# Performance work log

Hardware: AMD Instinct MI355X
Metric: run time of the kernel (lower is better)

The kernel has to match this reference:

```python
import jax, jax.numpy as jnp
import numpy as np

D_MODEL = 1024
H = 16
D_HEAD = D_MODEL // H
MASK_VAL = -1e30


def setup_inputs() -> dict:
    key = jax.random.key(0)
    ks = jax.random.split(key, 10)
    B, S = 2, 2048
    scale = 1.0 / np.sqrt(D_MODEL)
    return {
        "query": jax.random.normal(ks[0], (B, S, D_MODEL), jnp.float32),
        "key": jax.random.normal(ks[1], (B, S, D_MODEL), jnp.float32),
        "value": jax.random.normal(ks[2], (B, S, D_MODEL), jnp.float32),
        "mask": jax.random.randint(ks[3], (B, S, S), 0, 2) > 0,
        "Wq": jax.random.normal(ks[4], (D_MODEL, D_MODEL), jnp.float32) * scale,
        "bq": jnp.zeros((D_MODEL,), jnp.float32),
        "Wk": jax.random.normal(ks[5], (D_MODEL, D_MODEL), jnp.float32) * scale,
        "bk": jnp.zeros((D_MODEL,), jnp.float32),
        "Wv": jax.random.normal(ks[6], (D_MODEL, D_MODEL), jnp.float32) * scale,
        "bv": jnp.zeros((D_MODEL,), jnp.float32),
    }


def _split_heads(x, B, S):
    # [B,S,D] -> [B,H,S,Dh]
    return x.reshape(B, S, H, D_HEAD).transpose(0, 2, 1, 3)


def reference(query, key, value, mask, Wq, bq, Wk, bk, Wv, bv):
    B, S, _ = query.shape
    q = _split_heads(query @ Wq.T + bq, B, S)
    k = _split_heads(key @ Wk.T + bk, B, S)
    v = _split_heads(value @ Wv.T + bv, B, S)
    # scale by sqrt of per-head dim (query.size(-1) after split)
    q = q / jnp.sqrt(jnp.asarray(D_HEAD, q.dtype))
    scores = jnp.einsum("bhqd,bhkd->bhqk", q, k)
    scores = jnp.where(mask[:, None, :, :], MASK_VAL, scores)
    attn = jax.nn.softmax(scores, axis=-1)
    out = jnp.einsum("bhqk,bhkd->bhqd", attn, v)
    return out.transpose(0, 2, 1, 3).reshape(B, S, D_MODEL)
```

## Files before the change

### kernel.cpp

```cpp
#include <hip/hip_runtime.h>
#include <hip/hip_bf16.h>

#define D_MODEL 1024
#define NH 16
#define DH 64
#define S_LEN 2048
#define BATCH 2
#define QSCALE (0.125f * 1.44269504088896f)

#define KV_HSTRIDE (S_LEN * DH)
#define WS_V_OFF   (NH * KV_HSTRIDE)
#define KVB_WORDS  (2 * NH * KV_HSTRIDE)
#define MB_WORDS   ((S_LEN / 64) * S_LEN)
#define KTILE 128
#define NT (S_LEN / KTILE)
#define X_ELEMS (BATCH * S_LEN * D_MODEL)
#define W_ELEMS (D_MODEL * D_MODEL)
#define KSTR 88

typedef __attribute__((ext_vector_type(8))) short bf16x8;
typedef __attribute__((ext_vector_type(4))) float f32x4;

static __device__ inline unsigned short f2bf(float f) {
    union { float f; unsigned u; } v; v.f = f;
    unsigned r = v.u + 0x7fffu + ((v.u >> 16) & 1u);
    return (unsigned short)(r >> 16);
}
static __device__ inline unsigned cvt2(float a, float b) {
    union { __hip_bfloat162 h2; unsigned u; } cv;
    cv.h2 = __float22bfloat162_rn(make_float2(a, b));
    return cv.u;
}
static __device__ inline bf16x8 pack8(f32x4 a, f32x4 b) {
    union { bf16x8 v; unsigned u[4]; } r;
    r.u[0] = cvt2(a[0], a[1]); r.u[1] = cvt2(a[2], a[3]);
    r.u[2] = cvt2(b[0], b[1]); r.u[3] = cvt2(b[2], b[3]);
    return r.v;
}
static __device__ inline bf16x8 cvt8(const float* __restrict__ p) {
    return pack8(*(const f32x4*)p, *(const f32x4*)(p + 4));
}
static __device__ inline float exp2_fast(float x) {
#if __has_builtin(__builtin_amdgcn_exp2f)
    return __builtin_amdgcn_exp2f(x);
#else
    return exp2f(x);
#endif
}
static __device__ inline void gload_lds16(const unsigned short* __restrict__ g,
                                          unsigned short* l, int lane) {
#if __has_builtin(__builtin_amdgcn_global_load_lds)
    __builtin_amdgcn_global_load_lds(
        (const __attribute__((address_space(1))) void*)g,
        (__attribute__((address_space(3))) void*)l, 16, 0, 0);
#else
    *(bf16x8*)((char*)l + lane * 16) = *(const bf16x8*)g;
#endif
}
static __device__ inline int vperm(int s) {
    return (s & ~31) | ((s & 12) << 1) | ((s & 16) >> 2) | (s & 3);
}

__global__ __launch_bounds__(256) void cvt_kernel(
    const float* __restrict__ q, const float* __restrict__ k,
    const float* __restrict__ v,
    const float* __restrict__ Wq, const float* __restrict__ Wk,
    const float* __restrict__ Wv,
    unsigned short* __restrict__ xb, unsigned short* __restrict__ wb)
{
    const int by = blockIdx.y;
    const float* src;
    unsigned short* dst;
    int t;
    if (blockIdx.x < 1024) {
        src = by == 0 ? q : (by == 1 ? k : v);
        dst = xb + (size_t)by * X_ELEMS;
        t = blockIdx.x * 256 + threadIdx.x;
    } else {
        src = by == 0 ? Wq : (by == 1 ? Wk : Wv);
        dst = wb + (size_t)by * W_ELEMS;
        t = (blockIdx.x - 1024) * 256 + threadIdx.x;
    }
    const size_t o = (size_t)t * 16;
    *(bf16x8*)&dst[o]     = cvt8(src + o);
    *(bf16x8*)&dst[o + 8] = cvt8(src + o + 8);
}

__global__ __launch_bounds__(256) void pack_mask_kernel(
    const int* __restrict__ mask, unsigned long long* __restrict__ mbits,
    int b_base)
{
    const int w    = blockIdx.x * 4 + (threadIdx.x >> 6);
    const int lane = threadIdx.x & 63;
    const int b    = b_base + (w >> 16);
    const int rem  = w & 65535;
    const int kt   = rem >> 11;
    const int s    = rem & 2047;
    const int v = mask[((size_t)b * S_LEN + s) * S_LEN + kt * 64 + lane];
    const unsigned long long bits = __ballot(v != 0);
    if (lane == 0) mbits[w] = bits;
}

__global__ __launch_bounds__(256) void proj_v2_kernel(
    const unsigned short* __restrict__ xb, const unsigned short* __restrict__ wb,
    const float* __restrict__ bq, const float* __restrict__ bk,
    const float* __restrict__ bv,
    float* __restrict__ q_out, unsigned short* __restrict__ ws)
{
    const int bx = blockIdx.x;
    const int by = blockIdx.y;
    const int z  = by >> 3;
    const int c0 = (by & 7) * 128;

    const unsigned short* A  = xb + (size_t)z * X_ELEMS;
    const unsigned short* Bw = wb + (size_t)z * W_ELEMS;
    const float* bias = z == 0 ? bq : (z == 1 ? bk : bv);

    const int tid  = threadIdx.x;
    const int wave = tid >> 6;
    const int lane = tid & 63;
    const int quad = lane >> 4;
    const int l16  = lane & 15;
    const int m0   = (wave & 1) * 64;
    const int n0   = (wave >> 1) * 64;

    __shared__ __align__(16) unsigned short As[128 * 32];
    __shared__ __align__(16) unsigned short Bs[128 * 32];

    const int r_lo = wave * 16 + (lane >> 2);
    const int r_hi = (wave + 4) * 16 + (lane >> 2);
    const int segu = (lane & 3) * 8;
    const int row0 = bx * 128;

    f32x4 acc[4][4] = {};

    for (int kk = 0; kk < D_MODEL; kk += 32) {
        gload_lds16(A  + (size_t)(row0 + r_lo) * D_MODEL + kk + segu, &As[wave * 512], lane);
        gload_lds16(A  + (size_t)(row0 + r_hi) * D_MODEL + kk + segu, &As[(wave + 4) * 512], lane);
        gload_lds16(Bw + (size_t)(c0 + r_lo) * D_MODEL + kk + segu, &Bs[wave * 512], lane);
        gload_lds16(Bw + (size_t)(c0 + r_hi) * D_MODEL + kk + segu, &Bs[(wave + 4) * 512], lane);
        __syncthreads();

        bf16x8 af[4], bfr[4];
#pragma unroll
        for (int i = 0; i < 4; ++i)
            af[i] = *(const bf16x8*)&As[(m0 + i * 16 + l16) * 32 + quad * 8];
#pragma unroll
        for (int j = 0; j < 4; ++j)
            bfr[j] = *(const bf16x8*)&Bs[(n0 + j * 16 + l16) * 32 + quad * 8];
#pragma unroll
        for (int i = 0; i < 4; ++i)
#pragma unroll
            for (int j = 0; j < 4; ++j)
                acc[i][j] = __builtin_amdgcn_mfma_f32_16x16x32_bf16(
                    af[i], bfr[j], acc[i][j], 0, 0, 0);
        __syncthreads();
    }

#pragma unroll
    for (int j = 0; j < 4; ++j) {
        const int cl  = c0 + n0 + j * 16 + l16;
        const float bval = bias[cl];
        const int h  = cl >> 6;
        const int dh = cl & 63;
#pragma unroll
        for (int i = 0; i < 4; ++i) {
#pragma unroll
            for (int r = 0; r < 4; ++r) {
                const int row = row0 + m0 + i * 16 + quad * 4 + r;
                const float v = acc[i][j][r] + bval;
                if (z == 0) {
                    q_out[(size_t)row * D_MODEL + cl] = v * QSCALE;
                } else {
                    unsigned short* slab = ws + (size_t)(row >> 11) * KVB_WORDS;
                    const int s = row & 2047;
                    if (z == 1)
                        slab[(size_t)h * KV_HSTRIDE + s * DH + dh] = f2bf(v);
                    else
                        slab[WS_V_OFF + (size_t)h * KV_HSTRIDE + dh * S_LEN + vperm(s)] = f2bf(v);
                }
            }
        }
    }
}

__global__ __launch_bounds__(256) void proj_fb_kernel(
    const float* __restrict__ q_in, const float* __restrict__ k_in,
    const float* __restrict__ v_in,
    const float* __restrict__ Wq, const float* __restrict__ bq,
    const float* __restrict__ Wk, const float* __restrict__ bk,
    const float* __restrict__ Wv, const float* __restrict__ bv,
    float* __restrict__ q_out, unsigned short* __restrict__ ws, int b_base)
{
    const int bx = blockIdx.x;
    const int by = blockIdx.y;
    const int z  = by >> 3;
    const int c0 = (by & 7) * 128;

    const float* x    = z == 0 ? q_in : (z == 1 ? k_in : v_in);
    const float* W    = z == 0 ? Wq   : (z == 1 ? Wk   : Wv);
    const float* bias = z == 0 ? bq   : (z == 1 ? bk   : bv);

    const int tid  = threadIdx.x;
    const int wave = tid >> 6;
    const int lane = tid & 63;
    const int quad = lane >> 4;
    const int l16  = lane & 15;
    const int m0   = (wave & 1) * 64;
    const int n0   = (wave >> 1) * 64;

    __shared__ __align__(16) unsigned short As[128][40];
    __shared__ __align__(16) unsigned short Bs[128][40];

    const int srow = tid >> 1;
    const int kcol = (tid & 1) * 16;
    const int row0 = b_base * S_LEN + bx * 128;
    const float* ag = x + (size_t)(row0 + srow) * D_MODEL + kcol;
    const float* bg = W + (size_t)(c0 + srow) * D_MODEL + kcol;

    f32x4 acc[4][4] = {};

    for (int kk = 0; kk < D_MODEL; kk += 32) {
        {
            f32x4 a0 = *(const f32x4*)(ag + kk);
            f32x4 a1 = *(const f32x4*)(ag + kk + 4);
            f32x4 a2 = *(const f32x4*)(ag + kk + 8);
            f32x4 a3 = *(const f32x4*)(ag + kk + 12);
            f32x4 b0 = *(const f32x4*)(bg + kk);
            f32x4 b1 = *(const f32x4*)(bg + kk + 4);
            f32x4 b2 = *(const f32x4*)(bg + kk + 8);
            f32x4 b3 = *(const f32x4*)(bg + kk + 12);
            *(bf16x8*)&As[srow][kcol]     = pack8(a0, a1);
            *(bf16x8*)&As[srow][kcol + 8] = pack8(a2, a3);
            *(bf16x8*)&Bs[srow][kcol]     = pack8(b0, b1);
            *(bf16x8*)&Bs[srow][kcol + 8] = pack8(b2, b3);
        }
        __syncthreads();

        bf16x8 af[4], bfr[4];
#pragma unroll
        for (int i = 0; i < 4; ++i)
            af[i] = *(const bf16x8*)&As[m0 + i * 16 + l16][quad * 8];
#pragma unroll
        for (int j = 0; j < 4; ++j)
            bfr[j] = *(const bf16x8*)&Bs[n0 + j * 16 + l16][quad * 8];
#pragma unroll
        for (int i = 0; i < 4; ++i)
#pragma unroll
            for (int j = 0; j < 4; ++j)
                acc[i][j] = __builtin_amdgcn_mfma_f32_16x16x32_bf16(
                    af[i], bfr[j], acc[i][j], 0, 0, 0);
        __syncthreads();
    }

#pragma unroll
    for (int j = 0; j < 4; ++j) {
        const int cl  = c0 + n0 + j * 16 + l16;
        const float bval = bias[cl];
        const int h  = cl >> 6;
        const int dh = cl & 63;
#pragma unroll
        for (int i = 0; i < 4; ++i) {
#pragma unroll
            for (int r = 0; r < 4; ++r) {
                const int row = row0 + m0 + i * 16 + quad * 4 + r;
                const float v = acc[i][j][r] + bval;
                if (z == 0) {
                    q_out[(size_t)row * D_MODEL + cl] = v * QSCALE;
                } else {
                    const int b_rel = (row >> 11) - b_base;
                    const int s     = row & 2047;
                    unsigned short* slab = ws + (size_t)b_rel * KVB_WORDS;
                    if (z == 1)
                        slab[(size_t)h * KV_HSTRIDE + s * DH + dh] = f2bf(v);
                    else
                        slab[WS_V_OFF + (size_t)h * KV_HSTRIDE + dh * S_LEN + vperm(s)] = f2bf(v);
                }
            }
        }
    }
}

__global__ __launch_bounds__(256) void attn_kernel(
    const unsigned short* __restrict__ ws,
    const unsigned long long* __restrict__ mbits,
    const int* __restrict__ mask,
    float* __restrict__ out, int b_base, int use_bits)
{
    const int h     = blockIdx.x;
    const int qtile = blockIdx.y;
    const int bz    = blockIdx.z;
    const int b0    = b_base + bz;

    const unsigned short* K  = ws + (size_t)bz * KVB_WORDS + (size_t)h * KV_HSTRIDE;
    const unsigned short* Vg = K + WS_V_OFF;
    const unsigned long long* mb = mbits + (size_t)bz * MB_WORDS;

    const int tid  = threadIdx.x;
    const int wave = tid >> 6;
    const int lane = tid & 63;
    const int quad = lane >> 4;
    const int l16  = lane & 15;
    const int q0   = qtile * 128;

    __shared__ __align__(16) unsigned short Vt[64][136];
    __shared__ __align__(16) unsigned short Kt[128 * KSTR];

    bf16x8 aq0a, aq1a, aq0b, aq1b;
    {
        const float* qa =
            out + (size_t)(b0 * S_LEN + q0 + wave * 16 + l16) * D_MODEL + h * DH;
        const float* qb = qa + (size_t)64 * D_MODEL;
        aq0a = cvt8(qa + quad * 8);  aq1a = cvt8(qa + 32 + quad * 8);
        aq0b = cvt8(qb + quad * 8);  aq1b = cvt8(qb + 32 + quad * 8);
    }

    const int qg = q0 + wave * 16 + l16;
    float l_a = 0.f, l_b = 0.f;
    f32x4 o_a[4] = {}, o_b[4] = {};

    const int krow = tid >> 1, kc = (tid & 1) * 32;
    const int vrow = tid >> 2, vc = (tid & 3) * 32;
    bf16x8 kr[4], vr[4];
    {
        const unsigned short* kp = K + (size_t)krow * DH + kc;
        const unsigned short* vp = Vg + (size_t)vrow * S_LEN + vc;
#pragma unroll
        for (int i = 0; i < 4; ++i) {
            kr[i] = *(const bf16x8*)(kp + 8 * i);
            vr[i] = *(const bf16x8*)(vp + 8 * i);
        }
    }

    for (int kt = 0; kt < NT; ++kt) {
#pragma unroll
        for (int i = 0; i < 4; ++i) {
            *(bf16x8*)&Kt[krow * KSTR + kc + 8 * i] = kr[i];
            *(bf16x8*)&Vt[vrow][vc + 8 * i]         = vr[i];
        }
        __syncthreads();

        if (kt + 1 < NT) {
            const unsigned short* kp = K + (size_t)((kt + 1) * KTILE + krow) * DH + kc;
            const unsigned short* vp = Vg + (size_t)vrow * S_LEN + (kt + 1) * KTILE + vc;
#pragma unroll
            for (int i = 0; i < 4; ++i) {
                kr[i] = *(const bf16x8*)(kp + 8 * i);
                vr[i] = *(const bf16x8*)(vp + 8 * i);
            }
        }

        unsigned long long wm0a = 0ull, wm1a = 0ull, wm0b = 0ull, wm1b = 0ull;
        if (use_bits) {
            wm0a = mb[(size_t)(2 * kt) * S_LEN + qg] >> (quad * 4);
            wm1a = mb[(size_t)(2 * kt + 1) * S_LEN + qg] >> (quad * 4);
            wm0b = mb[(size_t)(2 * kt) * S_LEN + qg + 64] >> (quad * 4);
            wm1b = mb[(size_t)(2 * kt + 1) * S_LEN + qg + 64] >> (quad * 4);
        }

        bf16x8 af_a[4], af_b[4];
#pragma unroll
        for (int c = 0; c < 4; ++c) {
            f32x4 sa[2], sb[2];
#pragma unroll
            for (int j = 0; j < 2; ++j) {
                const int blk = 2 * c + j;
                const unsigned short* kb = &Kt[(blk * 16 + l16) * KSTR];
                bf16x8 k0 = *(const bf16x8*)&kb[quad * 8];
                bf16x8 k1 = *(const bf16x8*)&kb[32 + quad * 8];
                f32x4 z = {0.f, 0.f, 0.f, 0.f};
                sa[j] = __builtin_amdgcn_mfma_f32_16x16x32_bf16(k0, aq0a, z, 0, 0, 0);
                sa[j] = __builtin_amdgcn_mfma_f32_16x16x32_bf16(k1, aq1a, sa[j], 0, 0, 0);
                sb[j] = __builtin_amdgcn_mfma_f32_16x16x32_bf16(k0, aq0b, z, 0, 0, 0);
                sb[j] = __builtin_amdgcn_mfma_f32_16x16x32_bf16(k1, aq1b, sb[j], 0, 0, 0);
            }
#pragma unroll
            for (int j = 0; j < 2; ++j) {
                const int blk = 2 * c + j;
                const unsigned long long wa = (blk < 4) ? wm0a : wm1a;
                const unsigned long long wb = (blk < 4) ? wm0b : wm1b;
                const int sh = (blk & 3) * 16;
#pragma unroll
                for (int r = 0; r < 4; ++r) {
                    bool ma, mbk;
                    if (use_bits) {
                        ma  = (wa >> (sh + r)) & 1ull;
                        mbk = (wb >> (sh + r)) & 1ull;
                    } else {
                        const int kg = kt * KTILE + blk * 16 + quad * 4 + r;
                        ma  = mask[((size_t)(b0 * S_LEN) + qg) * S_LEN + kg] != 0;
                        mbk = mask[((size_t)(b0 * S_LEN) + qg + 64) * S_LEN + kg] != 0;
                    }
                    const float pa = ma  ? 0.0f : exp2_fast(sa[j][r]);
                    const float pb = mbk ? 0.0f : exp2_fast(sb[j][r]);
                    sa[j][r] = pa; l_a += pa;
                    sb[j][r] = pb; l_b += pb;
                }
            }
            {
                union { bf16x8 v; unsigned u[4]; } pk;
                pk.u[0] = cvt2(sa[0][0], sa[0][1]);
                pk.u[1] = cvt2(sa[0][2], sa[0][3]);
                pk.u[2] = cvt2(sa[1][0], sa[1][1]);
                pk.u[3] = cvt2(sa[1][2], sa[1][3]);
                af_a[c] = pk.v;
                pk.u[0] = cvt2(sb[0][0], sb[0][1]);
                pk.u[1] = cvt2(sb[0][2], sb[0][3]);
                pk.u[2] = cvt2(sb[1][0], sb[1][1]);
                pk.u[3] = cvt2(sb[1][2], sb[1][3]);
                af_b[c] = pk.v;
            }
        }

#pragma unroll
        for (int d = 0; d < 4; ++d) {
#pragma unroll
            for (int c = 0; c < 4; ++c) {
                bf16x8 bv = *(const bf16x8*)&Vt[d * 16 + l16][c * 32 + quad * 8];
                o_a[d] = __builtin_amdgcn_mfma_f32_16x16x32_bf16(af_a[c], bv, o_a[d], 0, 0, 0);
                o_b[d] = __builtin_amdgcn_mfma_f32_16x16x32_bf16(af_b[c], bv, o_b[d], 0, 0, 0);
            }
        }
        __syncthreads();
    }

    l_a += __shfl_xor(l_a, 16, 64);
    l_a += __shfl_xor(l_a, 32, 64);
    l_b += __shfl_xor(l_b, 16, 64);
    l_b += __shfl_xor(l_b, 32, 64);

#pragma unroll
    for (int r = 0; r < 4; ++r) {
        const float la = __shfl(l_a, quad * 4 + r, 64);
        const float lb = __shfl(l_b, quad * 4 + r, 64);
        const float ia = 1.0f / fmaxf(la, 1e-30f);
        const float ib = 1.0f / fmaxf(lb, 1e-30f);
        const int qgr = q0 + wave * 16 + quad * 4 + r;
#pragma unroll
        for (int d = 0; d < 4; ++d) {
            out[((size_t)(b0 * S_LEN) + qgr) * D_MODEL + h * DH + d * 16 + l16] =
                o_a[d][r] * ia;
            out[((size_t)(b0 * S_LEN) + qgr + 64) * D_MODEL + h * DH + d * 16 + l16] =
                o_b[d][r] * ib;
        }
    }
}

extern "C" void kernel_launch(void* const* d_in, const int* in_sizes, int n_in,
                              void* d_out, int out_size, void* d_ws, size_t ws_size,
                              hipStream_t stream) {
    const float* query = (const float*)d_in[0];
    const float* key   = (const float*)d_in[1];
    const float* value = (const float*)d_in[2];
    const int*   mask  = (const int*)d_in[3];
    const float* Wq    = (const float*)d_in[4];
    const float* bq    = (const float*)d_in[5];
    const float* Wk    = (const float*)d_in[6];
    const float* bk    = (const float*)d_in[7];
    const float* Wv    = (const float*)d_in[8];
    const float* bv    = (const float*)d_in[9];

    unsigned short* ws   = (unsigned short*)d_ws;
    float*          outp = (float*)d_out;

    const size_t KV_BYTES = (size_t)KVB_WORDS * 2;
    const size_t MB_BYTES = (size_t)MB_WORDS * 8;
    const size_t XB_BYTES = (size_t)3 * X_ELEMS * 2;
    const size_t WB_BYTES = (size_t)3 * W_ELEMS * 2;
    const size_t base2    = 2 * KV_BYTES + 2 * MB_BYTES;

    if (ws_size >= base2 + XB_BYTES + WB_BYTES) {
        unsigned long long* mbits = (unsigned long long*)(ws + 2 * KVB_WORDS);
        unsigned short* xb = ws + base2 / 2;
        unsigned short* wb = xb + (size_t)3 * X_ELEMS;
        cvt_kernel<<<dim3(1280, 3), 256, 0, stream>>>(
            query, key, value, Wq, Wk, Wv, xb, wb);
        proj_v2_kernel<<<dim3(32, 24), 256, 0, stream>>>(
            xb, wb, bq, bk, bv, outp, ws);
        pack_mask_kernel<<<dim3(2 * MB_WORDS / 4), 256, 0, stream>>>(mask, mbits, 0);
        attn_kernel<<<dim3(NH, S_LEN / 128, 2), 256, 0, stream>>>(
            ws, mbits, mask, outp, 0, 1);
    } else if (ws_size >= base2) {
        unsigned long long* mbits = (unsigned long long*)(ws + 2 * KVB_WORDS);
        proj_fb_kernel<<<dim3(32, 24), 256, 0, stream>>>(
            query, key, value, Wq, bq, Wk, bk, Wv, bv, outp, ws, 0);
        pack_mask_kernel<<<dim3(2 * MB_WORDS / 4), 256, 0, stream>>>(mask, mbits, 0);
        attn_kernel<<<dim3(NH, S_LEN / 128, 2), 256, 0, stream>>>(
            ws, mbits, mask, outp, 0, 1);
    } else if (ws_size >= KV_BYTES + MB_BYTES) {
        unsigned long long* mbits = (unsigned long long*)(ws + KVB_WORDS);
        for (int b0 = 0; b0 < BATCH; ++b0) {
            proj_fb_kernel<<<dim3(16, 24), 256, 0, stream>>>(
                query, key, value, Wq, bq, Wk, bk, Wv, bv, outp, ws, b0);
            pack_mask_kernel<<<dim3(MB_WORDS / 4), 256, 0, stream>>>(mask, mbits, b0);
            attn_kernel<<<dim3(NH, S_LEN / 128, 1), 256, 0, stream>>>(
                ws, mbits, mask, outp, b0, 1);
        }
    } else {
        for (int b0 = 0; b0 < BATCH; ++b0) {
            proj_fb_kernel<<<dim3(16, 24), 256, 0, stream>>>(
                query, key, value, Wq, bq, Wk, bk, Wv, bv, outp, ws, b0);
            attn_kernel<<<dim3(NH, S_LEN / 128, 1), 256, 0, stream>>>(
                ws, (const unsigned long long*)ws, mask, outp, b0, 0);
        }
    }
}
```

Before: 266.9 us.

## Double-buffer K/V tiles in LDS for attention kernel

Adds an attention kernel that keeps two K/V tile buffers in dynamic shared memory. Each iteration computes on the current buffer while the next tile is written to the other one, so only one barrier per tile is needed instead of two. The trade is double the LDS per block, which may lower occupancy, and it relies on the dynamic shared memory attribute call succeeding. The softmax also skips the running max and applies exp2 to scores directly.

```diff
diff --git a/kernel.cpp b/kernel.cpp
--- a/kernel.cpp
+++ b/kernel.cpp
@@ -17,6 +17,9 @@
 #define X_ELEMS (BATCH * S_LEN * D_MODEL)
 #define W_ELEMS (D_MODEL * D_MODEL)
 #define KSTR 88
+#define VSTR 136
+#define BUFW (128 * KSTR + 64 * VSTR)
+#define BUF_BYTES (BUFW * 2)
 
 typedef __attribute__((ext_vector_type(8))) short bf16x8;
 typedef __attribute__((ext_vector_type(4))) float f32x4;
@@ -281,7 +284,186 @@
     }
 }
 
-__global__ __launch_bounds__(256) void attn_kernel(
+__global__ __launch_bounds__(256) void attn_db_kernel(
+    const unsigned short* __restrict__ ws,
+    const unsigned long long* __restrict__ mbits,
+    float* __restrict__ out)
+{
+    const int h     = blockIdx.x;
+    const int qtile = blockIdx.y;
+    const int bz    = blockIdx.z;
+
+    const unsigned short* K  = ws + (size_t)bz * KVB_WORDS + (size_t)h * KV_HSTRIDE;
+    const unsigned short* Vg = K + WS_V_OFF;
+    const unsigned long long* mb = mbits + (size_t)bz * MB_WORDS;
+
+    const int tid  = threadIdx.x;
+    const int wave = tid >> 6;
+    const int lane = tid & 63;
+    const int quad = lane >> 4;
+    const int l16  = lane & 15;
+    const int q0   = qtile * 128;
+
+    extern __shared__ __align__(16) unsigned short lds[];
+
+    bf16x8 aq0a, aq1a, aq0b, aq1b;
+    {
+        const float* qa =
+            out + (size_t)(bz * S_LEN + q0 + wave * 16 + l16) * D_MODEL + h * DH;
+        const float* qb = qa + (size_t)64 * D_MODEL;
+        aq0a = cvt8(qa + quad * 8);  aq1a = cvt8(qa + 32 + quad * 8);
+        aq0b = cvt8(qb + quad * 8);  aq1b = cvt8(qb + 32 + quad * 8);
+    }
+
+    const int qg = q0 + wave * 16 + l16;
+    float l_a = 0.f, l_b = 0.f;
+    f32x4 o_a[4] = {}, o_b[4] = {};
+
+    const int krow = tid >> 1, kc = (tid & 1) * 32;
+    const int vrow = tid >> 2, vc = (tid & 3) * 32;
+    bf16x8 kr[4], vr[4];
+    {
+        const unsigned short* kp = K + (size_t)krow * DH + kc;
+        const unsigned short* vp = Vg + (size_t)vrow * S_LEN + vc;
+#pragma unroll
+        for (int i = 0; i < 4; ++i) {
+            kr[i] = *(const bf16x8*)(kp + 8 * i);
+            vr[i] = *(const bf16x8*)(vp + 8 * i);
+        }
+    }
+    unsigned long long wm0a = mb[qg] >> (quad * 4);
+    unsigned long long wm1a = mb[(size_t)S_LEN + qg] >> (quad * 4);
+    unsigned long long wm0b = mb[qg + 64] >> (quad * 4);
+    unsigned long long wm1b = mb[(size_t)S_LEN + qg + 64] >> (quad * 4);
+
+    {
+        unsigned short* Kt0 = lds;
+        unsigned short* Vt0 = lds + 128 * KSTR;
+#pragma unroll
+        for (int i = 0; i < 4; ++i) {
+            *(bf16x8*)&Kt0[krow * KSTR + kc + 8 * i] = kr[i];
+            *(bf16x8*)&Vt0[vrow * VSTR + vc + 8 * i] = vr[i];
+        }
+    }
+
+    for (int kt = 0; kt < NT; ++kt) {
+        __syncthreads();
+        unsigned short* Ktc = lds + (kt & 1) * BUFW;
+        unsigned short* Vtc = Ktc + 128 * KSTR;
+
+        if (kt + 1 < NT) {
+            const unsigned short* kp = K + (size_t)((kt + 1) * KTILE + krow) * DH + kc;
+            const unsigned short* vp = Vg + (size_t)vrow * S_LEN + (kt + 1) * KTILE + vc;
+#pragma unroll
+            for (int i = 0; i < 4; ++i) {
+                kr[i] = *(const bf16x8*)(kp + 8 * i);
+                vr[i] = *(const bf16x8*)(vp + 8 * i);
+            }
+        }
+        unsigned long long nm0a = 0ull, nm1a = 0ull, nm0b = 0ull, nm1b = 0ull;
+        if (kt + 1 < NT) {
+            nm0a = mb[(size_t)(2 * kt + 2) * S_LEN + qg] >> (quad * 4);
+            nm1a = mb[(size_t)(2 * kt + 3) * S_LEN + qg] >> (quad * 4);
+            nm0b = mb[(size_t)(2 * kt + 2) * S_LEN + qg + 64] >> (quad * 4);
+            nm1b = mb[(size_t)(2 * kt + 3) * S_LEN + qg + 64] >> (quad * 4);
+        }
+
+        bf16x8 af_a[4], af_b[4];
+#pragma unroll
+        for (int c = 0; c < 4; ++c) {
+            f32x4 sa[2], sb[2];
+            __builtin_amdgcn_s_setprio(1);
+#pragma unroll
+            for (int j = 0; j < 2; ++j) {
+                const int blk = 2 * c + j;
+                const unsigned short* kb = &Ktc[(blk * 16 + l16) * KSTR];
+                bf16x8 k0 = *(const bf16x8*)&kb[quad * 8];
+                bf16x8 k1 = *(const bf16x8*)&kb[32 + quad * 8];
+                f32x4 z = {0.f, 0.f, 0.f, 0.f};
+                sa[j] = __builtin_amdgcn_mfma_f32_16x16x32_bf16(k0, aq0a, z, 0, 0, 0);
+                sa[j] = __builtin_amdgcn_mfma_f32_16x16x32_bf16(k1, aq1a, sa[j], 0, 0, 0);
+                sb[j] = __builtin_amdgcn_mfma_f32_16x16x32_bf16(k0, aq0b, z, 0, 0, 0);
+                sb[j] = __builtin_amdgcn_mfma_f32_16x16x32_bf16(k1, aq1b, sb[j], 0, 0, 0);
+            }
+            __builtin_amdgcn_s_setprio(0);
+#pragma unroll
+            for (int j = 0; j < 2; ++j) {
+                const int blk = 2 * c + j;
+                const unsigned long long wa = (blk < 4) ? wm0a : wm1a;
+                const unsigned long long wb = (blk < 4) ? wm0b : wm1b;
+                const int sh = (blk & 3) * 16;
+#pragma unroll
+                for (int r = 0; r < 4; ++r) {
+                    const bool ma  = (wa >> (sh + r)) & 1ull;
+                    const bool mbk = (wb >> (sh + r)) & 1ull;
+                    const float pa = ma  ? 0.0f : exp2_fast(sa[j][r]);
+                    const float pb = mbk ? 0.0f : exp2_fast(sb[j][r]);
+                    sa[j][r] = pa; l_a += pa;
+                    sb[j][r] = pb; l_b += pb;
+                }
+            }
+            {
+                union { bf16x8 v; unsigned u[4]; } pk;
+                pk.u[0] = cvt2(sa[0][0], sa[0][1]);
+                pk.u[1] = cvt2(sa[0][2], sa[0][3]);
+                pk.u[2] = cvt2(sa[1][0], sa[1][1]);
+                pk.u[3] = cvt2(sa[1][2], sa[1][3]);
+                af_a[c] = pk.v;
+                pk.u[0] = cvt2(sb[0][0], sb[0][1]);
+                pk.u[1] = cvt2(sb[0][2], sb[0][3]);
+                pk.u[2] = cvt2(sb[1][0], sb[1][1]);
+                pk.u[3] = cvt2(sb[1][2], sb[1][3]);
+                af_b[c] = pk.v;
+            }
+        }
+
+        __builtin_amdgcn_s_setprio(1);
+#pragma unroll
+        for (int d = 0; d < 4; ++d) {
+#pragma unroll
+            for (int c = 0; c < 4; ++c) {
+                bf16x8 bv = *(const bf16x8*)&Vtc[(d * 16 + l16) * VSTR + c * 32 + quad * 8];
+                o_a[d] = __builtin_amdgcn_mfma_f32_16x16x32_bf16(af_a[c], bv, o_a[d], 0, 0, 0);
+                o_b[d] = __builtin_amdgcn_mfma_f32_16x16x32_bf16(af_b[c], bv, o_b[d], 0, 0, 0);
+            }
+        }
+        __builtin_amdgcn_s_setprio(0);
+
+        if (kt + 1 < NT) {
+            unsigned short* Ktn = lds + ((kt + 1) & 1) * BUFW;
+            unsigned short* Vtn = Ktn + 128 * KSTR;
+#pragma unroll
+            for (int i = 0; i < 4; ++i) {
+                *(bf16x8*)&Ktn[krow * KSTR + kc + 8 * i] = kr[i];
+                *(bf16x8*)&Vtn[vrow * VSTR + vc + 8 * i] = vr[i];
+            }
+        }
+        wm0a = nm0a; wm1a = nm1a; wm0b = nm0b; wm1b = nm1b;
+    }
+
+    l_a += __shfl_xor(l_a, 16, 64);
+    l_a += __shfl_xor(l_a, 32, 64);
+    l_b += __shfl_xor(l_b, 16, 64);
+    l_b += __shfl_xor(l_b, 32, 64);
+
+#pragma unroll
+    for (int r = 0; r < 4; ++r) {
+        const float la = __shfl(l_a, quad * 4 + r, 64);
+        const float lb = __shfl(l_b, quad * 4 + r, 64);
+        const float ia = 1.0f / fmaxf(la, 1e-30f);
+        const float ib = 1.0f / fmaxf(lb, 1e-30f);
+        const int qgr = q0 + wave * 16 + quad * 4 + r;
+#pragma unroll
+        for (int d = 0; d < 4; ++d) {
+            out[((size_t)(bz * S_LEN) + qgr) * D_MODEL + h * DH + d * 16 + l16] =
+                o_a[d][r] * ia;
+            out[((size_t)(bz * S_LEN) + qgr + 64) * D_MODEL + h * DH + d * 16 + l16] =
+                o_b[d][r] * ib;
+        }
+    }
+}
+
+__global__ __launch_bounds__(256) void attn_sb_kernel(
     const unsigned short* __restrict__ ws,
     const unsigned long long* __restrict__ mbits,
     const int* __restrict__ mask,
@@ -303,7 +485,7 @@
     const int l16  = lane & 15;
     const int q0   = qtile * 128;
 
-    __shared__ __align__(16) unsigned short Vt[64][136];
+    __shared__ __align__(16) unsigned short Vt[64][VSTR];
     __shared__ __align__(16) unsigned short Kt[128 * KSTR];
 
     bf16x8 aq0a, aq1a, aq0b, aq1b;
@@ -469,6 +651,14 @@
     const size_t WB_BYTES = (size_t)3 * W_ELEMS * 2;
     const size_t base2    = 2 * KV_BYTES + 2 * MB_BYTES;
 
+    static int db_ok = -1;
+    if (db_ok < 0) {
+        hipError_t e = hipFuncSetAttribute(
+            reinterpret_cast<const void*>(attn_db_kernel),
+            hipFuncAttributeMaxDynamicSharedMemorySize, 2 * BUF_BYTES);
+        db_ok = (e == hipSuccess) ? 1 : 0;
+    }
+
     if (ws_size >= base2 + XB_BYTES + WB_BYTES) {
         unsigned long long* mbits = (unsigned long long*)(ws + 2 * KVB_WORDS);
         unsigned short* xb = ws + base2 / 2;
@@ -478,29 +668,37 @@
         proj_v2_kernel<<<dim3(32, 24), 256, 0, stream>>>(
             xb, wb, bq, bk, bv, outp, ws);
         pack_mask_kernel<<<dim3(2 * MB_WORDS / 4), 256, 0, stream>>>(mask, mbits, 0);
-        attn_kernel<<<dim3(NH, S_LEN / 128, 2), 256, 0, stream>>>(
-            ws, mbits, mask, outp, 0, 1);
+        if (db_ok)
+            attn_db_kernel<<<dim3(NH, S_LEN / 128, 2), 256, 2 * BUF_BYTES, stream>>>(
+                ws, mbits, outp);
+        else
+            attn_sb_kernel<<<dim3(NH, S_LEN / 128, 2), 256, 0, stream>>>(
+                ws, mbits, mask, outp, 0, 1);
     } else if (ws_size >= base2) {
         unsigned long long* mbits = (unsigned long long*)(ws + 2 * KVB_WORDS);
         proj_fb_kernel<<<dim3(32, 24), 256, 0, stream>>>(
             query, key, value, Wq, bq, Wk, bk, Wv, bv, outp, ws, 0);
         pack_mask_kernel<<<dim3(2 * MB_WORDS / 4), 256, 0, stream>>>(mask, mbits, 0);
-        attn_kernel<<<dim3(NH, S_LEN / 128, 2), 256, 0, stream>>>(
-            ws, mbits, mask, outp, 0, 1);
+        if (db_ok)
+            attn_db_kernel<<<dim3(NH, S_LEN / 128, 2), 256, 2 * BUF_BYTES, stream>>>(
+                ws, mbits, outp);
+        else
+            attn_sb_kernel<<<dim3(NH, S_LEN / 128, 2), 256, 0, stream>>>(
+                ws, mbits, mask, outp, 0, 1);
     } else if (ws_size >= KV_BYTES + MB_BYTES) {
         unsigned long long* mbits = (unsigned long long*)(ws + KVB_WORDS);
         for (int b0 = 0; b0 < BATCH; ++b0) {
             proj_fb_kernel<<<dim3(16, 24), 256, 0, stream>>>(
                 query, key, value, Wq, bq, Wk, bk, Wv, bv, outp, ws, b0);
             pack_mask_kernel<<<dim3(MB_WORDS / 4), 256, 0, stream>>>(mask, mbits, b0);
-            attn_kernel<<<dim3(NH, S_LEN / 128, 1), 256, 0, stream>>>(
+            attn_sb_kernel<<<dim3(NH, S_LEN / 128, 1), 256, 0, stream>>>(
                 ws, mbits, mask, outp, b0, 1);
         }
     } else {
         for (int b0 = 0; b0 < BATCH; ++b0) {
             proj_fb_kernel<<<dim3(16, 24), 256, 0, stream>>>(
                 query, key, value, Wq, bq, Wk, bk, Wv, bv, outp, ws, b0);
-            attn_kernel<<<dim3(NH, S_LEN / 128, 1), 256, 0, stream>>>(
+            attn_sb_kernel<<<dim3(NH, S_LEN / 128, 1), 256, 0, stream>>>(
                 ws, (const unsigned long long*)ws, mask, outp, b0, 0);
         }
     }
```

New measurement: 253.2 us. 1.05x faster.
